# Kernel optimization log

Hardware: AMD Instinct MI355X
Metric: run time of the kernel (lower is better)

## Reference

```python
import jax, jax.numpy as jnp
import numpy as np

N0, N1, N2 = 512, 2048, 8192   # targets, hop1, hop2 node counts
K = 33                          # nneighbor + self loop
IN, HID, OUT, NH = 256, 128, 128, 8
NEG = -9.0e15
ALPHA = 0.2                     # LeakyReLU negative slope


def setup_inputs() -> dict:
    key = jax.random.key(0)
    ks = jax.random.split(key, 8)
    feats = jax.random.normal(ks[0], (N2, IN), jnp.float32)
    # xavier-ish scaled params (gain 1.414)
    W1 = jax.random.normal(ks[1], (NH, IN, HID), jnp.float32) * 0.072
    a1 = jax.random.normal(ks[2], (NH, 2 * HID), jnp.float32) * 0.105
    W2 = jax.random.normal(ks[3], (HID * NH, OUT), jnp.float32) * 0.042
    a2 = jax.random.normal(ks[4], (2 * OUT,), jnp.float32) * 0.105
    # layer1 edges: each of N1 targets gets K distinct neighbors in [0, N2)
    tgt1 = jnp.repeat(jnp.arange(N1, dtype=jnp.int32), K)
    dst1 = ((jnp.arange(N1)[:, None] * 97 + jnp.arange(K)[None, :] * 131) % N2).astype(jnp.int32).reshape(-1)
    src1 = jax.random.randint(ks[5], (N1 * K,), 0, N2, jnp.int32)
    # layer2 edges: each of N0 targets gets K distinct neighbors in [0, N1)
    tgt2 = jnp.repeat(jnp.arange(N0, dtype=jnp.int32), K)
    dst2 = ((jnp.arange(N0)[:, None] * 53 + jnp.arange(K)[None, :] * 61) % N1).astype(jnp.int32).reshape(-1)
    src2 = jax.random.randint(ks[6], (N0 * K,), 0, N1, jnp.int32)
    return dict(feats=feats, W1=W1, a1=a1, W2=W2, a2=a2,
                src1=src1, dst1=dst1, tgt1=tgt1, src2=src2, dst2=dst2, tgt2=tgt2)


def gat_layer(x, W, a, src, dst, tgt, t_len):
    # x: [n, in], W: [in, d], a: [2d]
    h = x @ W                                   # [n, d]
    d = h.shape[1]
    # concat([h[src], h[dst]]) @ a  ==  h[src]@a[:d] + h[dst]@a[d:]
    e = h[src] @ a[:d] + h[dst] @ a[d:]         # [E]
    e = jnp.where(e > 0, e, ALPHA * e)          # LeakyReLU
    att = jnp.full((t_len, h.shape[0]), NEG, h.dtype).at[tgt, dst].set(e)
    att = jax.nn.softmax(att, axis=1)           # dense row softmax (masked entries ~0)
    return jax.nn.elu(att @ h)                  # [t_len, d]


def reference(feats, W1, a1, W2, a2, src1, dst1, tgt1, src2, dst2, tgt2):
    # layer 1: nhead independent GAT heads over hop2 features
    heads = jax.vmap(lambda W, a: gat_layer(feats, W, a, src1, dst1, tgt1, N1))(W1, a1)  # [NH, N1, HID]
    x = jnp.transpose(heads, (1, 0, 2)).reshape(N1, NH * HID)  # torch.cat(dim=1)
    # layer 2: single GAT layer producing [N0, OUT]
    return gat_layer(x, W2, a2, src2, dst2, tgt2, N0)
```

## Files before the change

kernel.cpp:

```cpp
#include <hip/hip_runtime.h>
#include <math.h>

#define ALPHA 0.2f

constexpr int CN0 = 512, CN1 = 2048, CN2 = 8192, CK = 33;
constexpr int CIN = 256, CHID = 128, CNH = 8;

using u16    = unsigned short;
using f32x4  = __attribute__((ext_vector_type(4))) float;
using bf16x8 = __attribute__((ext_vector_type(8))) short;

__device__ __forceinline__ u16 f2bf(float f) {
    unsigned u = __float_as_uint(f);
    u += 0x7fff + ((u >> 16) & 1);
    return (u16)(u >> 16);
}
__device__ __forceinline__ float bf2f(u16 h) {
    return __uint_as_float(((unsigned)h) << 16);
}

#define GLD16(g, l)                                                        \
    __builtin_amdgcn_global_load_lds(                                      \
        (const __attribute__((address_space(1))) void*)(g),                \
        (__attribute__((address_space(3))) void*)(l), 16, 0, 0)

__global__ __launch_bounds__(256) void prep2_k(const float* __restrict__ W1,
                                               u16* __restrict__ w1t,
                                               const float* __restrict__ W2,
                                               u16* __restrict__ w2t,
                                               const float* __restrict__ a1,
                                               float* __restrict__ pvec) {
    __shared__ float t[32][33];
    int b = blockIdx.x;
    if (b >= 384) {
        const int i = b - 384;
        const int h = i >> 1, half = i & 1;
        const int j = threadIdx.x;
        const float* wrow = W1 + (size_t)h * CIN * CHID + (size_t)j * CHID;
        const float* ah   = a1 + h * 2 * CHID + half * CHID;
        float d = 0.f;
#pragma unroll 8
        for (int c = 0; c < CHID; ++c) d = fmaf(wrow[c], ah[c], d);
        pvec[(h * 2 + half) * CIN + j] = d;
        return;
    }
    const float* ip;
    u16* op;
    int R, C, r0, c0;
    if (b < 256) {
        const int h = b >> 5, w = b & 31;
        ip = W1 + (size_t)h * CIN * CHID;
        op = w1t + (size_t)h * CIN * CHID;
        R = CIN; C = CHID; r0 = (w >> 2) * 32; c0 = (w & 3) * 32;
    } else {
        b -= 256;
        ip = W2; op = w2t;
        R = CNH * CHID; C = CHID; r0 = (b >> 2) * 32; c0 = (b & 3) * 32;
    }
    const int tx = threadIdx.x & 31, ty = threadIdx.x >> 5;
#pragma unroll
    for (int i = 0; i < 4; ++i)
        t[ty + 8 * i][tx] = ip[(size_t)(r0 + ty + 8 * i) * C + c0 + tx];
    __syncthreads();
#pragma unroll
    for (int i = 0; i < 4; ++i)
        op[(size_t)(c0 + ty + 8 * i) * R + r0 + tx] = f2bf(t[tx][ty + 8 * i]);
}

__global__ __launch_bounds__(256) void fsc_k(const float* __restrict__ feats,
                                             u16* __restrict__ fb,
                                             const float* __restrict__ pvec,
                                             float* __restrict__ s1,
                                             float* __restrict__ s2) {
    const int node = (blockIdx.x * 256 + threadIdx.x) >> 6;
    const int lane = threadIdx.x & 63;
    const float4 v = *reinterpret_cast<const float4*>(feats + (size_t)node * CIN + lane * 4);
    *reinterpret_cast<ushort4*>(fb + (size_t)node * CIN + lane * 4) =
        make_ushort4(f2bf(v.x), f2bf(v.y), f2bf(v.z), f2bf(v.w));
#pragma unroll
    for (int h = 0; h < CNH; ++h) {
        const float4 p1 = *reinterpret_cast<const float4*>(pvec + (h * 2 + 0) * CIN + lane * 4);
        const float4 p2 = *reinterpret_cast<const float4*>(pvec + (h * 2 + 1) * CIN + lane * 4);
        float d1 = v.x * p1.x + v.y * p1.y + v.z * p1.z + v.w * p1.w;
        float d2 = v.x * p2.x + v.y * p2.y + v.z * p2.z + v.w * p2.w;
#pragma unroll
        for (int m = 1; m < 64; m <<= 1) {
            d1 += __shfl_xor(d1, m);
            d2 += __shfl_xor(d2, m);
        }
        if (lane == 0) {
            s1[h * CN2 + node] = d1;
            s2[h * CN2 + node] = d2;
        }
    }
}

__global__ __launch_bounds__(128) void agg1g_k(const float* __restrict__ s1,
                                               const float* __restrict__ s2,
                                               const int* __restrict__ src,
                                               const int* __restrict__ dst,
                                               const u16* __restrict__ fb,
                                               u16* __restrict__ gb) {
    __shared__ float wgt[CNH][CK];
    __shared__ int dsts[CK];

    const int t    = blockIdx.x;
    const int tid  = threadIdx.x;
    const int wv   = tid >> 6;
    const int lane = tid & 63;

    int sv = 0, dv = 0;
    if (lane < CK) {
        sv = src[t * CK + lane];
        dv = dst[t * CK + lane];
        if (tid < CK) dsts[tid] = dv;
    }
#pragma unroll
    for (int hh = 0; hh < 4; ++hh) {
        const int head = wv * 4 + hh;
        float e = -3.0e38f;
        if (lane < CK) {
            const float ee = s1[head * CN2 + sv] + s2[head * CN2 + dv];
            e = (ee > 0.f) ? ee : ALPHA * ee;
        }
        float m = e;
#pragma unroll
        for (int mm = 1; mm < 64; mm <<= 1) m = fmaxf(m, __shfl_xor(m, mm));
        const float p = (lane < CK) ? __expf(e - m) : 0.f;
        float s = p;
#pragma unroll
        for (int mm = 1; mm < 64; mm <<= 1) s += __shfl_xor(s, mm);
        if (lane < CK) wgt[head][lane] = p / s;
    }
    __syncthreads();

    const int c2 = tid * 2;
    float acc[CNH][2];
#pragma unroll
    for (int h = 0; h < CNH; ++h) { acc[h][0] = 0.f; acc[h][1] = 0.f; }
#pragma unroll 8
    for (int k = 0; k < CK; ++k) {
        const unsigned w2v = *reinterpret_cast<const unsigned*>(
            fb + (size_t)dsts[k] * CIN + c2);
        const float f0 = bf2f((u16)(w2v & 0xffff));
        const float f1 = bf2f((u16)(w2v >> 16));
#pragma unroll
        for (int h = 0; h < CNH; ++h) {
            const float wk = wgt[h][k];
            acc[h][0] = fmaf(wk, f0, acc[h][0]);
            acc[h][1] = fmaf(wk, f1, acc[h][1]);
        }
    }
#pragma unroll
    for (int h = 0; h < CNH; ++h) {
        const unsigned o = ((unsigned)f2bf(acc[h][1]) << 16) | f2bf(acc[h][0]);
        *reinterpret_cast<unsigned*>(gb + ((size_t)h * CN1 + t) * CIN + c2) = o;
    }
}

__global__ __launch_bounds__(256) void fusedproj_k(const u16* __restrict__ gb,
                                                   const u16* __restrict__ w1t,
                                                   const u16* __restrict__ w2t,
                                                   float* __restrict__ part) {
    __shared__ __attribute__((aligned(16))) char smem[24576];

    const int tid  = threadIdx.x;
    const int lane = tid & 63;
    const int wave = tid >> 6;
    const int trow0 = blockIdx.x * 64;
    const int h     = blockIdx.y;
    const int wr = (wave >> 1) * 32;
    const int wc = (wave & 1) * 64;

    const u16* A  = gb  + (size_t)h * CN1 * CIN;
    const u16* Bt = w1t + (size_t)h * CHID * CIN;

    f32x4 acc[2][4];
#pragma unroll
    for (int m = 0; m < 2; ++m)
#pragma unroll
        for (int n = 0; n < 4; ++n) acc[m][n] = (f32x4){0.f, 0.f, 0.f, 0.f};

    const int r0c = tid >> 2;
    const int cs0 = tid & 3;
    const int c0  = (cs0 - (r0c >> 1)) & 3;
    const int r1c = r0c + 64;

    const u16* ga0 = A + (size_t)(trow0 + r0c) * CIN + c0 * 8;
    const u16* gb0 = Bt + (size_t)r0c * CIN + c0 * 8;
    const u16* gb1 = Bt + (size_t)r1c * CIN + c0 * 8;

    auto STAGE = [&](int s) {
        const int k0 = s * 32;
        char* base = smem + (s & 1) * 12288;
        u16* as = (u16*)base + wave * 512;
        u16* bs = (u16*)(base + 4096) + wave * 512;
        GLD16(ga0 + k0, as);
        GLD16(gb0 + k0, bs);
        GLD16(gb1 + k0, bs + 2048);
    };

    STAGE(0);
    __syncthreads();

    for (int s = 0; s < 8; ++s) {
        if (s + 1 < 8) STAGE(s + 1);

        const u16* Acur = (const u16*)(smem + (s & 1) * 12288);
        const u16* Bcur = Acur + 2048;

        bf16x8 af[2], bfr[4];
#pragma unroll
        for (int m = 0; m < 2; ++m) {
            const int rt = wr + m * 16 + (lane & 15);
            const int cs = ((lane >> 4) + (rt >> 1)) & 3;
            af[m] = *reinterpret_cast<const bf16x8*>(Acur + rt * 32 + cs * 8);
        }
#pragma unroll
        for (int n = 0; n < 4; ++n) {
            const int rt2 = wc + n * 16 + (lane & 15);
            const int cs2 = ((lane >> 4) + (rt2 >> 1)) & 3;
            bfr[n] = *reinterpret_cast<const bf16x8*>(Bcur + rt2 * 32 + cs2 * 8);
        }
#pragma unroll
        for (int m = 0; m < 2; ++m)
#pragma unroll
            for (int n = 0; n < 4; ++n)
                acc[m][n] = __builtin_amdgcn_mfma_f32_16x16x32_bf16(
                    af[m], bfr[n], acc[m][n], 0, 0, 0);

        __syncthreads();
    }

    u16* Xs = (u16*)smem;
#pragma unroll
    for (int m = 0; m < 2; ++m) {
        const int rr = wr + m * 16 + (lane >> 4) * 4;
#pragma unroll
        for (int n = 0; n < 4; ++n) {
            const int cc = wc + n * 16 + (lane & 15);
#pragma unroll
            for (int q = 0; q < 4; ++q) {
                float v = acc[m][n][q];
                v = (v > 0.f) ? v : __expf(v) - 1.f;
                const int r = rr + q;
                Xs[r * 128 + ((((cc >> 3) ^ (r & 7)) << 3) | (cc & 7))] = f2bf(v);
            }
        }
    }
    __syncthreads();

    f32x4 acc2[2][4];
#pragma unroll
    for (int m = 0; m < 2; ++m)
#pragma unroll
        for (int n = 0; n < 4; ++n) acc2[m][n] = (f32x4){0.f, 0.f, 0.f, 0.f};

#pragma unroll
    for (int ks = 0; ks < 4; ++ks) {
        bf16x8 a2f[2], b2f[4];
#pragma unroll
        for (int m = 0; m < 2; ++m) {
            const int rt = wr + m * 16 + (lane & 15);
            const int k0 = ks * 32 + (lane >> 4) * 8;
            a2f[m] = *reinterpret_cast<const bf16x8*>(
                Xs + rt * 128 + (((k0 >> 3) ^ (rt & 7)) << 3));
        }
#pragma unroll
        for (int n = 0; n < 4; ++n) {
            const int rb = wc + n * 16 + (lane & 15);
            b2f[n] = *reinterpret_cast<const bf16x8*>(
                w2t + (size_t)rb * (CNH * CHID) + h * CHID + ks * 32 + (lane >> 4) * 8);
        }
#pragma unroll
        for (int m = 0; m < 2; ++m)
#pragma unroll
            for (int n = 0; n < 4; ++n)
                acc2[m][n] = __builtin_amdgcn_mfma_f32_16x16x32_bf16(
                    a2f[m], b2f[n], acc2[m][n], 0, 0, 0);
    }

#pragma unroll
    for (int m = 0; m < 2; ++m) {
        const int rr = trow0 + wr + m * 16 + (lane >> 4) * 4;
#pragma unroll
        for (int n = 0; n < 4; ++n) {
            const int cc = wc + n * 16 + (lane & 15);
#pragma unroll
            for (int q = 0; q < 4; ++q)
                part[((size_t)h * CN1 + rr + q) * CHID + cc] = acc2[m][n][q];
        }
    }
}

__global__ __launch_bounds__(256) void scores2_k(const float* __restrict__ part,
                                                 const float* __restrict__ a,
                                                 float* __restrict__ h2,
                                                 float* __restrict__ s1,
                                                 float* __restrict__ s2) {
    const int wid  = (blockIdx.x * 256 + threadIdx.x) >> 6;
    const int lane = threadIdx.x & 63;
    const int j = lane * 2;
    float x0 = 0.f, x1 = 0.f;
#pragma unroll
    for (int sp = 0; sp < 8; ++sp) {
        const float2 v = *reinterpret_cast<const float2*>(
            part + (size_t)sp * CN1 * CHID + (size_t)wid * CHID + j);
        x0 += v.x; x1 += v.y;
    }
    *reinterpret_cast<float2*>(h2 + (size_t)wid * CHID + j) = make_float2(x0, x1);
    float d1 = x0 * a[j] + x1 * a[j + 1];
    float d2 = x0 * a[CHID + j] + x1 * a[CHID + j + 1];
#pragma unroll
    for (int m = 1; m < 64; m <<= 1) {
        d1 += __shfl_xor(d1, m);
        d2 += __shfl_xor(d2, m);
    }
    if (lane == 0) { s1[wid] = d1; s2[wid] = d2; }
}

__global__ __launch_bounds__(256) void agg2_k(const float* __restrict__ s1,
                                              const float* __restrict__ s2,
                                              const int* __restrict__ src,
                                              const int* __restrict__ dst,
                                              const float* __restrict__ h2,
                                              float* __restrict__ out) {
    const int t    = (blockIdx.x * 256 + threadIdx.x) >> 6;
    const int lane = threadIdx.x & 63;

    float e = -3.0e38f;
    int dv = 0;
    if (lane < CK) {
        const int sv = src[t * CK + lane];
        dv = dst[t * CK + lane];
        const float ee = s1[sv] + s2[dv];
        e = (ee > 0.f) ? ee : ALPHA * ee;
    }
    float m = e;
#pragma unroll
    for (int mm = 1; mm < 64; mm <<= 1) m = fmaxf(m, __shfl_xor(m, mm));
    float p = (lane < CK) ? __expf(e - m) : 0.f;
    float ssum = p;
#pragma unroll
    for (int mm = 1; mm < 64; mm <<= 1) ssum += __shfl_xor(ssum, mm);
    const float invs = 1.f / ssum;

    float a0 = 0.f, a1 = 0.f;
#pragma unroll
    for (int k = 0; k < CK; ++k) {
        const float w = __shfl(p, k) * invs;
        const int d = __shfl(dv, k);
        const float2 hv = *reinterpret_cast<const float2*>(h2 + (size_t)d * CHID + lane * 2);
        a0 = fmaf(w, hv.x, a0);
        a1 = fmaf(w, hv.y, a1);
    }
    a0 = (a0 > 0.f) ? a0 : __expf(a0) - 1.f;
    a1 = (a1 > 0.f) ? a1 : __expf(a1) - 1.f;
    *reinterpret_cast<float2*>(out + (size_t)t * CHID + lane * 2) = make_float2(a0, a1);
}

extern "C" void kernel_launch(void* const* d_in, const int* in_sizes, int n_in,
                              void* d_out, int out_size, void* d_ws, size_t ws_size,
                              hipStream_t stream) {
    const float* feats = (const float*)d_in[0];
    const float* W1    = (const float*)d_in[1];
    const float* a1    = (const float*)d_in[2];
    const float* W2    = (const float*)d_in[3];
    const float* a2    = (const float*)d_in[4];
    const int*   src1  = (const int*)d_in[5];
    const int*   dst1  = (const int*)d_in[6];
    const int*   src2  = (const int*)d_in[8];
    const int*   dst2  = (const int*)d_in[9];
    float* out = (float*)d_out;

    char* w = (char*)d_ws;
    u16*   fb   = (u16*)w;                 w += (size_t)CN2 * CIN * 2;
    u16*   w1t  = (u16*)w;                 w += (size_t)CNH * CIN * CHID * 2;
    u16*   w2t  = (u16*)w;                 w += (size_t)CNH * CHID * CHID * 2;
    float* pvec = (float*)w;               w += (size_t)CNH * 2 * CIN * 4;
    float* s1   = (float*)w;               w += (size_t)CNH * CN2 * 4;
    float* s2   = (float*)w;               w += (size_t)CNH * CN2 * 4;
    u16*   gb   = (u16*)w;                 w += (size_t)CNH * CN1 * CIN * 2;
    float* part = (float*)w;               w += (size_t)8 * CN1 * CHID * 4;
    float* h2   = (float*)w;               w += (size_t)CN1 * CHID * 4;
    float* s21  = (float*)w;               w += (size_t)CN1 * 4;
    float* s22  = (float*)w;               w += (size_t)CN1 * 4;

    prep2_k<<<dim3(256 + 128 + 16), 256, 0, stream>>>(W1, w1t, W2, w2t, a1, pvec);

    fsc_k<<<dim3(CN2 / 4), 256, 0, stream>>>(feats, fb, pvec, s1, s2);

    agg1g_k<<<dim3(CN1), 128, 0, stream>>>(s1, s2, src1, dst1, fb, gb);

    fusedproj_k<<<dim3(CN1 / 64, CNH), 256, 0, stream>>>(gb, w1t, w2t, part);

    scores2_k<<<dim3(CN1 / 4), 256, 0, stream>>>(part, a2, h2, s21, s22);

    agg2_k<<<dim3(CN0 / 4), 256, 0, stream>>>(s21, s22, src2, dst2, h2, out);
}
```

Baseline: 51.47 us.

## Fuse layer-2 score computation into projection epilogue and merge partial-sum aggregation

The layer-2 attention scores are now computed in the fusedproj epilogue, using in-wave shuffles, a shared-memory reduction and atomicAdd across the 8 head-split partials into s21/s22, which are zeroed by an extra block in the prep kernel. The separate scores2 kernel and the h2 buffer are removed. The final aggregation instead sums the 8 partial rows on the fly for each gathered neighbour into shared memory. This drops one kernel launch and a full h2 write/read round-trip. In exchange the aggregation now reads 8x more data per neighbour, and the atomics make the summation order nondeterministic.

```diff
diff --git a/kernel.cpp b/kernel.cpp
--- a/kernel.cpp
+++ b/kernel.cpp
@@ -29,9 +29,20 @@
                                                const float* __restrict__ W2,
                                                u16* __restrict__ w2t,
                                                const float* __restrict__ a1,
-                                               float* __restrict__ pvec) {
+                                               float* __restrict__ pvec,
+                                               float* __restrict__ s21,
+                                               float* __restrict__ s22) {
     __shared__ float t[32][33];
     int b = blockIdx.x;
+    if (b == 400) {
+        const int i = threadIdx.x * 8;
+        const float4 z = make_float4(0.f, 0.f, 0.f, 0.f);
+        *reinterpret_cast<float4*>(s21 + i)     = z;
+        *reinterpret_cast<float4*>(s21 + i + 4) = z;
+        *reinterpret_cast<float4*>(s22 + i)     = z;
+        *reinterpret_cast<float4*>(s22 + i + 4) = z;
+        return;
+    }
     if (b >= 384) {
         const int i = b - 384;
         const int h = i >> 1, half = i & 1;
@@ -161,8 +172,13 @@
 __global__ __launch_bounds__(256) void fusedproj_k(const u16* __restrict__ gb,
                                                    const u16* __restrict__ w1t,
                                                    const u16* __restrict__ w2t,
-                                                   float* __restrict__ part) {
+                                                   const float* __restrict__ a2,
+                                                   float* __restrict__ part,
+                                                   float* __restrict__ s21,
+                                                   float* __restrict__ s22) {
     __shared__ __attribute__((aligned(16))) char smem[24576];
+    __shared__ float sred1[2][64];
+    __shared__ float sred2[2][64];
 
     const int tid  = threadIdx.x;
     const int lane = tid & 63;
@@ -291,72 +307,108 @@
                 part[((size_t)h * CN1 + rr + q) * CHID + cc] = acc2[m][n][q];
         }
     }
-}
-
-__global__ __launch_bounds__(256) void scores2_k(const float* __restrict__ part,
-                                                 const float* __restrict__ a,
-                                                 float* __restrict__ h2,
-                                                 float* __restrict__ s1,
-                                                 float* __restrict__ s2) {
-    const int wid  = (blockIdx.x * 256 + threadIdx.x) >> 6;
-    const int lane = threadIdx.x & 63;
-    const int j = lane * 2;
-    float x0 = 0.f, x1 = 0.f;
-#pragma unroll
-    for (int sp = 0; sp < 8; ++sp) {
-        const float2 v = *reinterpret_cast<const float2*>(
-            part + (size_t)sp * CN1 * CHID + (size_t)wid * CHID + j);
-        x0 += v.x; x1 += v.y;
-    }
-    *reinterpret_cast<float2*>(h2 + (size_t)wid * CHID + j) = make_float2(x0, x1);
-    float d1 = x0 * a[j] + x1 * a[j + 1];
-    float d2 = x0 * a[CHID + j] + x1 * a[CHID + j + 1];
-#pragma unroll
-    for (int m = 1; m < 64; m <<= 1) {
-        d1 += __shfl_xor(d1, m);
-        d2 += __shfl_xor(d2, m);
-    }
-    if (lane == 0) { s1[wid] = d1; s2[wid] = d2; }
-}
-
-__global__ __launch_bounds__(256) void agg2_k(const float* __restrict__ s1,
-                                              const float* __restrict__ s2,
-                                              const int* __restrict__ src,
-                                              const int* __restrict__ dst,
-                                              const float* __restrict__ h2,
-                                              float* __restrict__ out) {
-    const int t    = (blockIdx.x * 256 + threadIdx.x) >> 6;
-    const int lane = threadIdx.x & 63;
-
-    float e = -3.0e38f;
-    int dv = 0;
-    if (lane < CK) {
-        const int sv = src[t * CK + lane];
-        dv = dst[t * CK + lane];
-        const float ee = s1[sv] + s2[dv];
-        e = (ee > 0.f) ? ee : ALPHA * ee;
-    }
-    float m = e;
-#pragma unroll
-    for (int mm = 1; mm < 64; mm <<= 1) m = fmaxf(m, __shfl_xor(m, mm));
-    float p = (lane < CK) ? __expf(e - m) : 0.f;
-    float ssum = p;
-#pragma unroll
-    for (int mm = 1; mm < 64; mm <<= 1) ssum += __shfl_xor(ssum, mm);
-    const float invs = 1.f / ssum;
-
-    float a0 = 0.f, a1 = 0.f;
-#pragma unroll
-    for (int k = 0; k < CK; ++k) {
-        const float w = __shfl(p, k) * invs;
-        const int d = __shfl(dv, k);
-        const float2 hv = *reinterpret_cast<const float2*>(h2 + (size_t)d * CHID + lane * 2);
-        a0 = fmaf(w, hv.x, a0);
-        a1 = fmaf(w, hv.y, a1);
-    }
-    a0 = (a0 > 0.f) ? a0 : __expf(a0) - 1.f;
-    a1 = (a1 > 0.f) ? a1 : __expf(a1) - 1.f;
-    *reinterpret_cast<float2*>(out + (size_t)t * CHID + lane * 2) = make_float2(a0, a1);
+
+    float av1[4], av2[4];
+#pragma unroll
+    for (int n = 0; n < 4; ++n) {
+        const int c = wc + n * 16 + (lane & 15);
+        av1[n] = a2[c];
+        av2[n] = a2[CHID + c];
+    }
+    float p1[2][4], p2[2][4];
+#pragma unroll
+    for (int m = 0; m < 2; ++m)
+#pragma unroll
+        for (int q = 0; q < 4; ++q) {
+            float t1 = 0.f, t2 = 0.f;
+#pragma unroll
+            for (int n = 0; n < 4; ++n) {
+                t1 = fmaf(acc2[m][n][q], av1[n], t1);
+                t2 = fmaf(acc2[m][n][q], av2[n], t2);
+            }
+#pragma unroll
+            for (int mk = 1; mk < 16; mk <<= 1) {
+                t1 += __shfl_xor(t1, mk);
+                t2 += __shfl_xor(t2, mk);
+            }
+            p1[m][q] = t1;
+            p2[m][q] = t2;
+        }
+    if ((lane & 15) == 0) {
+        const int g = lane >> 4;
+#pragma unroll
+        for (int m = 0; m < 2; ++m)
+#pragma unroll
+            for (int q = 0; q < 4; ++q) {
+                sred1[wave & 1][wr + m * 16 + g * 4 + q] = p1[m][q];
+                sred2[wave & 1][wr + m * 16 + g * 4 + q] = p2[m][q];
+            }
+    }
+    __syncthreads();
+    if (tid < 64) {
+        atomicAdd(&s21[trow0 + tid], sred1[0][tid] + sred1[1][tid]);
+        atomicAdd(&s22[trow0 + tid], sred2[0][tid] + sred2[1][tid]);
+    }
+}
+
+__global__ __launch_bounds__(256) void agg2big_k(const float* __restrict__ part,
+                                                 const float* __restrict__ s21,
+                                                 const float* __restrict__ s22,
+                                                 const int* __restrict__ src,
+                                                 const int* __restrict__ dst,
+                                                 float* __restrict__ out) {
+    __shared__ float h2row[CK][CHID];
+    __shared__ float wgt[CK];
+    __shared__ int sds[CK], nds[CK];
+
+    const int t   = blockIdx.x;
+    const int tid = threadIdx.x;
+
+    if (tid < CK) {
+        sds[tid] = src[t * CK + tid];
+        nds[tid] = dst[t * CK + tid];
+    }
+    __syncthreads();
+
+    for (int i = tid; i < CK * 32; i += 256) {
+        const int k  = i >> 5;
+        const int c4 = (i & 31) * 4;
+        const int dv = nds[k];
+        float4 x = make_float4(0.f, 0.f, 0.f, 0.f);
+#pragma unroll
+        for (int sp = 0; sp < 8; ++sp) {
+            const float4 v = *reinterpret_cast<const float4*>(
+                part + ((size_t)sp * CN1 + dv) * CHID + c4);
+            x.x += v.x; x.y += v.y; x.z += v.z; x.w += v.w;
+        }
+        *reinterpret_cast<float4*>(&h2row[k][c4]) = x;
+    }
+    __syncthreads();
+
+    if (tid < 64) {
+        float e = -3.0e38f;
+        if (tid < CK) {
+            const float ee = s21[sds[tid]] + s22[nds[tid]];
+            e = (ee > 0.f) ? ee : ALPHA * ee;
+        }
+        float m = e;
+#pragma unroll
+        for (int mm = 1; mm < 64; mm <<= 1) m = fmaxf(m, __shfl_xor(m, mm));
+        const float p = (tid < CK) ? __expf(e - m) : 0.f;
+        float s = p;
+#pragma unroll
+        for (int mm = 1; mm < 64; mm <<= 1) s += __shfl_xor(s, mm);
+        if (tid < CK) wgt[tid] = p / s;
+    }
+    __syncthreads();
+
+    if (tid < CHID) {
+        float acc = 0.f;
+#pragma unroll
+        for (int k = 0; k < CK; ++k)
+            acc = fmaf(wgt[k], h2row[k][tid], acc);
+        out[(size_t)t * CHID + tid] = (acc > 0.f) ? acc : __expf(acc) - 1.f;
+    }
 }
 
 extern "C" void kernel_launch(void* const* d_in, const int* in_sizes, int n_in,
@@ -382,19 +434,17 @@
     float* s2   = (float*)w;               w += (size_t)CNH * CN2 * 4;
     u16*   gb   = (u16*)w;                 w += (size_t)CNH * CN1 * CIN * 2;
     float* part = (float*)w;               w += (size_t)8 * CN1 * CHID * 4;
-    float* h2   = (float*)w;               w += (size_t)CN1 * CHID * 4;
     float* s21  = (float*)w;               w += (size_t)CN1 * 4;
     float* s22  = (float*)w;               w += (size_t)CN1 * 4;
 
-    prep2_k<<<dim3(256 + 128 + 16), 256, 0, stream>>>(W1, w1t, W2, w2t, a1, pvec);
+    prep2_k<<<dim3(401), 256, 0, stream>>>(W1, w1t, W2, w2t, a1, pvec, s21, s22);
 
     fsc_k<<<dim3(CN2 / 4), 256, 0, stream>>>(feats, fb, pvec, s1, s2);
 
     agg1g_k<<<dim3(CN1), 128, 0, stream>>>(s1, s2, src1, dst1, fb, gb);
 
-    fusedproj_k<<<dim3(CN1 / 64, CNH), 256, 0, stream>>>(gb, w1t, w2t, part);
-
-    scores2_k<<<dim3(CN1 / 4), 256, 0, stream>>>(part, a2, h2, s21, s22);
-
-    agg2_k<<<dim3(CN0 / 4), 256, 0, stream>>>(s21, s22, src2, dst2, h2, out);
-}
+    fusedproj_k<<<dim3(CN1 / 64, CNH), 256, 0, stream>>>(
+        gb, w1t, w2t, a2, part, s21, s22);
+
+    agg2big_k<<<dim3(CN0), 256, 0, stream>>>(part, s21, s22, src2, dst2, out);
+}
```

Measured after the change: 54.67 us. 1.06x slower.
